# Optimization experiments

Measured on AMD Instinct MI355X. Metric: run time of the kernel, lower is better.

The kernel has to match this reference:

```python
import jax, jax.numpy as jnp
import numpy as np

B, S, L = 4, 1024, 128
H, D = 16, 64            # num_attention_heads, attention_head_size
HID = H * D              # 1024
MAX_POS = 1024


def setup_inputs() -> dict:
    key = jax.random.key(0)
    ks = jax.random.split(key, 12)
    sc = 1.0 / np.sqrt(HID)
    return {
        "hidden_states": jax.random.normal(ks[0], (B, S, HID), jnp.float32),
        "attention_mask": jnp.zeros((B, 1, 1, S), jnp.float32),
        "instruct_hidden_states": jax.random.normal(ks[1], (B, L, HID), jnp.float32),
        "instruct_attention_mask": jnp.zeros((B, 1, 1, L), jnp.float32),
        "Wq": jax.random.normal(ks[2], (HID, HID), jnp.float32) * sc,
        "bq": jnp.zeros((HID,), jnp.float32),
        "Wk": jax.random.normal(ks[3], (HID, HID), jnp.float32) * sc,
        "bk": jnp.zeros((HID,), jnp.float32),
        "Wv": jax.random.normal(ks[4], (HID, HID), jnp.float32) * sc,
        "bv": jnp.zeros((HID,), jnp.float32),
        "gate": jnp.zeros((1, H, 1, 1), jnp.float32),
        "dist_emb": jax.random.normal(ks[5], (2 * MAX_POS - 1, D), jnp.float32) * 0.02,
    }


def _heads(x):
    # [B,T,HID] -> [B,H,T,D]
    b, t, _ = x.shape
    return x.reshape(b, t, H, D).transpose(0, 2, 1, 3)


def reference(hidden_states, attention_mask, instruct_hidden_states,
              instruct_attention_mask, Wq, bq, Wk, bk, Wv, bv, gate, dist_emb):
    inv_sqrt_d = 1.0 / jnp.sqrt(jnp.asarray(D, hidden_states.dtype))

    q = _heads(hidden_states @ Wq + bq)            # [B,H,S,D]
    k = _heads(hidden_states @ Wk + bk)
    v = _heads(hidden_states @ Wv + bv)
    ik = _heads(instruct_hidden_states @ Wk + bk)  # [B,H,L,D]
    iv = _heads(instruct_hidden_states @ Wv + bv)

    scores = jnp.einsum('bhld,bhrd->bhlr', q, k)   # [B,H,S,S]

    # relative_key_query positional scores
    pos = jnp.arange(S)
    dist_idx = pos[:, None] - pos[None, :] + MAX_POS - 1   # [S,S]
    pe = dist_emb[dist_idx]                                # [S,S,D]
    scores = scores + jnp.einsum('bhld,lrd->bhlr', q, pe) \
                    + jnp.einsum('bhrd,lrd->bhlr', k, pe)

    scores = scores * inv_sqrt_d + attention_mask
    probs = jax.nn.softmax(scores, axis=-1)
    ctx = jnp.einsum('bhlr,bhrd->bhld', probs, v)          # [B,H,S,D]

    # gated instruction attention
    iscores = jnp.einsum('bhld,bhrd->bhlr', q, ik) * inv_sqrt_d + instruct_attention_mask
    iprobs = jax.nn.softmax(iscores, axis=-1)
    ictx = jnp.einsum('bhlr,bhrd->bhld', iprobs, iv)
    ctx = ctx + jnp.tanh(gate) * ictx

    # [B,H,S,D] -> [B,S,HID]
    return ctx.transpose(0, 2, 1, 3).reshape(B, S, HID)
```

## Files before the change

### kernel.cpp

```cpp
#include <hip/hip_runtime.h>
#include <cmath>

#define NB 4
#define NH 16
#define SD 64
#define SEQ 1024
#define ILEN 128
#define HIDDIM 1024

#define N_HID (NB*SEQ*HIDDIM)
#define N_INS (NB*ILEN*HIDDIM)
#define N_E_SRC (2047*SD)
#define N_E   (2048*SD)
#define N_W   (HIDDIM*HIDDIM)

typedef short bf8 __attribute__((ext_vector_type(8)));
typedef short bf4 __attribute__((ext_vector_type(4)));
typedef float f4  __attribute__((ext_vector_type(4)));

#define MFMA(a,b,c) __builtin_amdgcn_mfma_f32_16x16x32_bf16(a,b,c,0,0,0)

__device__ __forceinline__ float bf2f(short s) {
    unsigned u = ((unsigned)(unsigned short)s) << 16;
    return __uint_as_float(u);
}
__device__ __forceinline__ short f2bf(float x) {
    unsigned u = __float_as_uint(x);
    u = (u + 0x7FFFu + ((u >> 16) & 1u)) >> 16;
    return (short)u;
}
__device__ __forceinline__ short f2bf_t(float x) {
    return (short)(__float_as_uint(x) >> 16);
}

__global__ __launch_bounds__(256) void cast_flat(
    const float* __restrict__ hid, const float* __restrict__ ins,
    const float* __restrict__ E, short* __restrict__ ws)
{
    int i = (blockIdx.x * 256 + threadIdx.x) * 4;
    short* dhid = ws;
    short* dins = ws + N_HID;
    short* dE   = ws + N_HID + N_INS;
    if (i < N_HID) {
        float4 v = *(const float4*)&hid[i];
        bf4 o; o[0]=f2bf(v.x); o[1]=f2bf(v.y); o[2]=f2bf(v.z); o[3]=f2bf(v.w);
        *(bf4*)&dhid[i] = o;
    } else if (i < N_HID + N_INS) {
        int j = i - N_HID;
        float4 v = *(const float4*)&ins[j];
        bf4 o; o[0]=f2bf(v.x); o[1]=f2bf(v.y); o[2]=f2bf(v.z); o[3]=f2bf(v.w);
        *(bf4*)&dins[j] = o;
    } else {
        int j = i - N_HID - N_INS;
        if (j < N_E) {
            bf4 o;
            if (j < N_E_SRC) {
                float4 v = *(const float4*)&E[j];
                o[0]=f2bf(v.x); o[1]=f2bf(v.y); o[2]=f2bf(v.z); o[3]=f2bf(v.w);
            } else {
                o[0]=0; o[1]=0; o[2]=0; o[3]=0;
            }
            *(bf4*)&dE[j] = o;
        }
    }
}

__global__ __launch_bounds__(256) void cast_wt(
    const float* __restrict__ Wq, const float* __restrict__ Wk,
    const float* __restrict__ Wv, short* __restrict__ dstbase)
{
    const float* W = (blockIdx.z==0) ? Wq : (blockIdx.z==1) ? Wk : Wv;
    short* dst = dstbase + (size_t)blockIdx.z * N_W;
    const int k0 = blockIdx.y*64, n0 = blockIdx.x*64;
    __shared__ float st[64][65];
    const int tid = threadIdx.x;
    #pragma unroll
    for (int rep=0; rep<4; rep++) {
        int u = tid + rep*256;
        int row = u >> 4, col = (u & 15) * 4;
        float4 v = *(const float4*)&W[(size_t)(k0+row)*HIDDIM + n0 + col];
        st[row][col+0]=v.x; st[row][col+1]=v.y; st[row][col+2]=v.z; st[row][col+3]=v.w;
    }
    __syncthreads();
    #pragma unroll
    for (int rep=0; rep<4; rep++) {
        int u = tid + rep*256;
        int nrow = u >> 4, kc = (u & 15) * 4;
        bf4 o;
        #pragma unroll
        for (int j=0;j<4;j++) o[j] = f2bf(st[kc+j][nrow]);
        *(bf4*)&dst[(size_t)(n0+nrow)*HIDDIM + k0 + kc] = o;
    }
}

__global__ __launch_bounds__(256) void proj_mfma(
    const short* __restrict__ hidb, const short* __restrict__ insb,
    const short* __restrict__ WTall,
    const float* __restrict__ bq, const float* __restrict__ bk, const float* __restrict__ bv,
    short* __restrict__ qo, short* __restrict__ ko, short* __restrict__ vTo,
    short* __restrict__ iko, short* __restrict__ ivTo)
{
    const int z = blockIdx.z;
    const int bx = blockIdx.x, by = blockIdx.y;
    if (z==1 && (bx>=16 || by>=4)) return;
    const short* X = z ? insb : hidb;
    const int T   = z ? ILEN : SEQ;
    const int tsh = z ? 7 : 10;
    const int zoff= z ? 1024 : 0;
    const int m0 = by*128, n0 = bx*128;

    __shared__ short Xs[128*72];
    __shared__ short Ws[128*72];

    const int tid=threadIdx.x, w=tid>>6, lane=tid&63, quad=lane>>4, nl=lane&15;
    const int wr = w>>1, wc = w&1;

    f4 acc[4][4];
    #pragma unroll
    for (int ti=0;ti<4;ti++)
      #pragma unroll
      for (int tj=0;tj<4;tj++) { acc[ti][tj][0]=0.f; acc[ti][tj][1]=0.f; acc[ti][tj][2]=0.f; acc[ti][tj][3]=0.f; }

    for (int k0=0; k0<HIDDIM; k0+=64) {
        __syncthreads();
        #pragma unroll
        for (int rep=0; rep<4; rep++) {
            int u = tid + rep*256;
            int row = u >> 3, ch = u & 7;
            *(uint4*)&Xs[row*72 + ch*8] = *(const uint4*)&X[(size_t)(m0+row)*HIDDIM + k0 + ch*8];
            *(uint4*)&Ws[row*72 + ch*8] = *(const uint4*)&WTall[(size_t)(zoff+n0+row)*HIDDIM + k0 + ch*8];
        }
        __syncthreads();
        bf8 a[4][2], b[4][2];
        #pragma unroll
        for (int ti=0;ti<4;ti++)
          #pragma unroll
          for (int s=0;s<2;s++)
            a[ti][s] = *(const bf8*)&Xs[(64*wr + 16*ti + nl)*72 + s*32 + quad*8];
        #pragma unroll
        for (int tj=0;tj<4;tj++)
          #pragma unroll
          for (int s=0;s<2;s++)
            b[tj][s] = *(const bf8*)&Ws[(64*wc + 16*tj + nl)*72 + s*32 + quad*8];
        #pragma unroll
        for (int ti=0;ti<4;ti++)
          #pragma unroll
          for (int tj=0;tj<4;tj++)
            #pragma unroll
            for (int s=0;s<2;s++)
              acc[ti][tj] = MFMA(a[ti][s], b[tj][s], acc[ti][tj]);
    }

    #pragma unroll
    for (int tj=0;tj<4;tj++) {
        const int n = n0 + 64*wc + 16*tj + nl;
        const int nn = n & 1023;
        const int h = nn >> 6, d = nn & 63;
        float bias; short* outp; int mode;
        if (z==0) {
            if (n < 1024)      { bias = bq[nn]; outp = qo;  mode=0; }
            else if (n < 2048) { bias = bk[nn]; outp = ko;  mode=0; }
            else               { bias = bv[nn]; outp = vTo; mode=1; }
        } else {
            if (n < 1024)      { bias = bk[nn]; outp = iko;  mode=0; }
            else               { bias = bv[nn]; outp = ivTo; mode=1; }
        }
        #pragma unroll
        for (int ti=0;ti<4;ti++) {
            const int mb = m0 + 64*wr + 16*ti + quad*4;
            const int bb = mb >> tsh, tt = mb & (T-1);
            if (mode) {
                bf4 o;
                #pragma unroll
                for (int i=0;i<4;i++) o[i] = f2bf(acc[ti][tj][i] + bias);
                *(bf4*)&outp[((size_t)(bb*NH + h)*SD + d)*T + tt] = o;
            } else {
                #pragma unroll
                for (int i=0;i<4;i++)
                    outp[((size_t)(bb*NH + h)*T + tt + i)*SD + d] = f2bf(acc[ti][tj][i] + bias);
            }
        }
    }
}

__global__ __launch_bounds__(256,2) void attn_mfma(
    const short* __restrict__ qg, const short* __restrict__ kg, const short* __restrict__ vTg,
    const short* __restrict__ ikg, const short* __restrict__ ivTg,
    const float* __restrict__ mask, const float* __restrict__ imask,
    const float* __restrict__ gate, const short* __restrict__ Ebf,
    float* __restrict__ out)
{
    const int l0 = blockIdx.x * 64, h = blockIdx.y, b = blockIdx.z;
    const int tid = threadIdx.x, w = tid>>6, lane = tid&63, quad = lane>>4, nl = lane&15;

    __shared__ short ksh[64*72];
    __shared__ short vts[64*72];
    __shared__ short es [128*72];
    __shared__ short qeT[128*68];
    __shared__ short keT[128*68];
    __shared__ short ps [64*72];
    __shared__ float maskS[64];

    const size_t bh = (size_t)(b*NH + h);
    const short* kbase   = kg   + bh*SEQ*SD;
    const short* vTbase  = vTg  + bh*SD*SEQ;
    const short* ikbase  = ikg  + bh*ILEN*SD;
    const short* ivTbase = ivTg + bh*SD*ILEN;

    bf8 aq[2];
    {
        const short* qrow = qg + (bh*SEQ + l0 + 16*w + nl)*SD;
        #pragma unroll
        for (int s=0;s<2;s++) aq[s] = *(const bf8*)&qrow[s*32 + quad*8];
    }

    f4 o1[4], o2[4];
    float m1[4], l1[4], m2[4], l2[4];
    #pragma unroll
    for (int t=0;t<4;t++) {
        o1[t][0]=0.f;o1[t][1]=0.f;o1[t][2]=0.f;o1[t][3]=0.f;
        o2[t][0]=0.f;o2[t][1]=0.f;o2[t][2]=0.f;o2[t][3]=0.f;
        m1[t]=-1e30f; l1[t]=0.f; m2[t]=-1e30f; l2[t]=0.f;
    }

    for (int r0=0; r0<SEQ; r0+=64) {
        const int jb = l0 - r0 + 960;
        __syncthreads();
        #pragma unroll
        for (int rep=0; rep<2; rep++) {
            int u = tid + rep*256;
            int row = u >> 3, ch = u & 7;
            *(uint4*)&ksh[row*72 + ch*8] = *(const uint4*)&kbase[(size_t)(r0+row)*SD + ch*8];
            *(uint4*)&vts[row*72 + ch*8] = *(const uint4*)&vTbase[(size_t)row*SEQ + r0 + ch*8];
        }
        if (r0 == 0) {
            #pragma unroll
            for (int rep=0; rep<4; rep++) {
                int u = tid + rep*256;
                int roff = u >> 3, ch = u & 7;
                int g = jb + roff;
                *(uint4*)&es[(g & 127)*72 + ch*8] = *(const uint4*)&Ebf[(size_t)g*SD + ch*8];
            }
        } else {
            #pragma unroll
            for (int rep=0; rep<2; rep++) {
                int u = tid + rep*256;
                int roff = u >> 3, ch = u & 7;
                int g = jb + roff;
                *(uint4*)&es[(g & 127)*72 + ch*8] = *(const uint4*)&Ebf[(size_t)g*SD + ch*8];
            }
        }
        if (tid < 64) maskS[tid] = mask[b*SEQ + r0 + tid];
        __syncthreads();

        bf8 ak[2];
        #pragma unroll
        for (int s=0;s<2;s++) ak[s] = *(const bf8*)&ksh[(16*w+nl)*72 + s*32 + quad*8];
        f4 sc[4];
        #pragma unroll
        for (int t=0;t<4;t++) { sc[t][0]=0.f; sc[t][1]=0.f; sc[t][2]=0.f; sc[t][3]=0.f; }
        #pragma unroll
        for (int t=0;t<4;t++)
            #pragma unroll
            for (int s=0;s<2;s++) {
                bf8 bk = *(const bf8*)&ksh[(16*t+nl)*72 + s*32 + quad*8];
                sc[t] = MFMA(aq[s], bk, sc[t]);
            }
        f4 qe[5], ke[5];
        #pragma unroll
        for (int j=0;j<5;j++) {
            qe[j][0]=0.f;qe[j][1]=0.f;qe[j][2]=0.f;qe[j][3]=0.f;
            ke[j][0]=0.f;ke[j][1]=0.f;ke[j][2]=0.f;ke[j][3]=0.f;
        }
        #pragma unroll
        for (int j=0;j<5;j++) {
            const int sq = (jb + 16*(w+j)   + nl) & 127;
            const int sk = (jb + 16*(3-w+j) + nl) & 127;
            #pragma unroll
            for (int s=0;s<2;s++) {
                bf8 beq = *(const bf8*)&es[sq*72 + s*32 + quad*8];
                bf8 bek = *(const bf8*)&es[sk*72 + s*32 + quad*8];
                qe[j] = MFMA(aq[s], beq, qe[j]);
                ke[j] = MFMA(ak[s], bek, ke[j]);
            }
        }
        #pragma unroll
        for (int j=0;j<5;j++) {
            bf4 pq, pk;
            #pragma unroll
            for (int i=0;i<4;i++) { pq[i]=f2bf_t(qe[j][i]); pk[i]=f2bf_t(ke[j][i]); }
            *(bf4*)&qeT[(16*(w+j)+nl)*68 + 16*w + quad*4]   = pq;
            *(bf4*)&keT[(16*(3-w+j)+nl)*68 + 16*w + quad*4] = pk;
        }
        __syncthreads();

        float sval[4][4];
        #pragma unroll
        for (int t=0;t<4;t++) {
            const int ri = 16*t + nl;
            const float mk = maskS[ri];
            #pragma unroll
            for (int i=0;i<4;i++) {
                const int li = 16*w + quad*4 + i;
                const int c = li - ri + 63;
                float add = bf2f(qeT[c*68 + li]) + bf2f(keT[c*68 + ri]);
                sval[i][t] = (sc[t][i] + add)*0.125f + mk;
            }
        }
        short pbf[4][4];
        #pragma unroll
        for (int i=0;i<4;i++) {
            float mx = fmaxf(fmaxf(sval[i][0],sval[i][1]), fmaxf(sval[i][2],sval[i][3]));
            #pragma unroll
            for (int off=1; off<16; off<<=1) mx = fmaxf(mx, __shfl_xor(mx, off));
            const float mn = fmaxf(m1[i], mx);
            const float alpha = __expf(m1[i]-mn);
            m1[i] = mn;
            float rs = 0.f;
            #pragma unroll
            for (int t=0;t<4;t++) {
                float p = __expf(sval[i][t]-mn);
                pbf[i][t] = f2bf(p);
                rs += p;
            }
            #pragma unroll
            for (int off=1; off<16; off<<=1) rs += __shfl_xor(rs, off);
            l1[i] = l1[i]*alpha + rs;
            #pragma unroll
            for (int t=0;t<4;t++) o1[t][i] *= alpha;
        }
        #pragma unroll
        for (int i=0;i<4;i++) {
            const int li = 16*w + quad*4 + i;
            #pragma unroll
            for (int t=0;t<4;t++) ps[li*72 + 16*t + nl] = pbf[i][t];
        }
        #pragma unroll
        for (int s=0;s<2;s++) {
            bf8 ap = *(const bf8*)&ps[(16*w+nl)*72 + s*32 + quad*8];
            #pragma unroll
            for (int t=0;t<4;t++) {
                bf8 bv = *(const bf8*)&vts[(16*t+nl)*72 + s*32 + quad*8];
                o1[t] = MFMA(ap, bv, o1[t]);
            }
        }
    }

    for (int r0=0; r0<ILEN; r0+=64) {
        __syncthreads();
        #pragma unroll
        for (int rep=0; rep<2; rep++) {
            int u = tid + rep*256;
            int row = u >> 3, ch = u & 7;
            *(uint4*)&ksh[row*72 + ch*8] = *(const uint4*)&ikbase[(size_t)(r0+row)*SD + ch*8];
            *(uint4*)&vts[row*72 + ch*8] = *(const uint4*)&ivTbase[(size_t)row*ILEN + r0 + ch*8];
        }
        __syncthreads();

        f4 sc[4];
        #pragma unroll
        for (int t=0;t<4;t++) { sc[t][0]=0.f; sc[t][1]=0.f; sc[t][2]=0.f; sc[t][3]=0.f; }
        #pragma unroll
        for (int t=0;t<4;t++)
            #pragma unroll
            for (int s=0;s<2;s++) {
                bf8 bk = *(const bf8*)&ksh[(16*t+nl)*72 + s*32 + quad*8];
                sc[t] = MFMA(aq[s], bk, sc[t]);
            }
        float sval[4][4];
        #pragma unroll
        for (int t=0;t<4;t++) {
            const float mk = imask[b*ILEN + r0 + 16*t + nl];
            #pragma unroll
            for (int i=0;i<4;i++) sval[i][t] = sc[t][i]*0.125f + mk;
        }
        short pbf[4][4];
        #pragma unroll
        for (int i=0;i<4;i++) {
            float mx = fmaxf(fmaxf(sval[i][0],sval[i][1]), fmaxf(sval[i][2],sval[i][3]));
            #pragma unroll
            for (int off=1; off<16; off<<=1) mx = fmaxf(mx, __shfl_xor(mx, off));
            const float mn = fmaxf(m2[i], mx);
            const float alpha = __expf(m2[i]-mn);
            m2[i] = mn;
            float rs = 0.f;
            #pragma unroll
            for (int t=0;t<4;t++) {
                float p = __expf(sval[i][t]-mn);
                pbf[i][t] = f2bf(p);
                rs += p;
            }
            #pragma unroll
            for (int off=1; off<16; off<<=1) rs += __shfl_xor(rs, off);
            l2[i] = l2[i]*alpha + rs;
            #pragma unroll
            for (int t=0;t<4;t++) o2[t][i] *= alpha;
        }
        #pragma unroll
        for (int i=0;i<4;i++) {
            const int li = 16*w + quad*4 + i;
            #pragma unroll
            for (int t=0;t<4;t++) ps[li*72 + 16*t + nl] = pbf[i][t];
        }
        #pragma unroll
        for (int s=0;s<2;s++) {
            bf8 ap = *(const bf8*)&ps[(16*w+nl)*72 + s*32 + quad*8];
            #pragma unroll
            for (int t=0;t<4;t++) {
                bf8 bv = *(const bf8*)&vts[(16*t+nl)*72 + s*32 + quad*8];
                o2[t] = MFMA(ap, bv, o2[t]);
            }
        }
    }

    const float tg = tanhf(gate[h]);
    #pragma unroll
    for (int i=0;i<4;i++) {
        const int l = l0 + 16*w + quad*4 + i;
        const float inv1 = 1.0f/l1[i], inv2 = 1.0f/l2[i];
        #pragma unroll
        for (int t=0;t<4;t++) {
            const int d = 16*t + nl;
            out[((size_t)(b*SEQ + l)*NH + h)*SD + d] = o1[t][i]*inv1 + tg*(o2[t][i]*inv2);
        }
    }
}

extern "C" void kernel_launch(void* const* d_in, const int* in_sizes, int n_in,
                              void* d_out, int out_size, void* d_ws, size_t ws_size,
                              hipStream_t stream) {
    const float* hidden  = (const float*)d_in[0];
    const float* mask    = (const float*)d_in[1];
    const float* ihidden = (const float*)d_in[2];
    const float* imask   = (const float*)d_in[3];
    const float* Wq   = (const float*)d_in[4];
    const float* bq   = (const float*)d_in[5];
    const float* Wk   = (const float*)d_in[6];
    const float* bk   = (const float*)d_in[7];
    const float* Wv   = (const float*)d_in[8];
    const float* bv   = (const float*)d_in[9];
    const float* gate = (const float*)d_in[10];
    const float* dist = (const float*)d_in[11];
    float* out = (float*)d_out;

    short* ws = (short*)d_ws;
    const size_t OFF_INS = N_HID;
    const size_t OFF_E   = OFF_INS + N_INS;
    const size_t OFF_WT  = OFF_E + N_E;
    const size_t OFF_Q   = OFF_WT + 3*(size_t)N_W;
    const size_t OFF_K   = OFF_Q + N_HID;
    const size_t OFF_VT  = OFF_K + N_HID;
    const size_t OFF_IK  = OFF_VT + N_HID;
    const size_t OFF_IVT = OFF_IK + N_INS;

    cast_flat<<<4736, 256, 0, stream>>>(hidden, ihidden, dist, ws);
    cast_wt<<<dim3(16,16,3), 256, 0, stream>>>(Wq, Wk, Wv, ws + OFF_WT);
    proj_mfma<<<dim3(24,32,2), 256, 0, stream>>>(
        ws, ws + OFF_INS, ws + OFF_WT,
        bq, bk, bv,
        ws + OFF_Q, ws + OFF_K, ws + OFF_VT, ws + OFF_IK, ws + OFF_IVT);
    attn_mfma<<<dim3(16,16,4), 256, 0, stream>>>(
        ws + OFF_Q, ws + OFF_K, ws + OFF_VT, ws + OFF_IK, ws + OFF_IVT,
        mask, imask, gate, ws + OFF_E, out);
}
```

Before: 277.6 us.

## Gather query-position scores via lane shuffles and alias LDS buffers to cut shared memory

The query-side relative-position term is now taken straight from MFMA accumulator registers with cross-lane shuffles, so the qeT shared-memory transpose buffer is no longer written or read. The probability buffers reuse the ksh and es regions, and the attention mask is loaded from global memory into registers, which removes maskS. Together these shrink LDS use per block, which may allow more resident blocks, and cut LDS traffic. The cost is extra shuffle and select instructions, and buffer aliasing that depends on the existing barrier ordering being correct. The key-side term now uses round-to-nearest bf16 conversion instead of truncation.

Measured after the change: 275.2 us. Within noise of the previous version (-0.9%).

```diff
diff --git a/kernel.cpp b/kernel.cpp
--- a/kernel.cpp
+++ b/kernel.cpp
@@ -28,9 +28,6 @@
     unsigned u = __float_as_uint(x);
     u = (u + 0x7FFFu + ((u >> 16) & 1u)) >> 16;
     return (short)u;
-}
-__device__ __forceinline__ short f2bf_t(float x) {
-    return (short)(__float_as_uint(x) >> 16);
 }
 
 __global__ __launch_bounds__(256) void cast_flat(
@@ -193,13 +190,12 @@
     const int l0 = blockIdx.x * 64, h = blockIdx.y, b = blockIdx.z;
     const int tid = threadIdx.x, w = tid>>6, lane = tid&63, quad = lane>>4, nl = lane&15;
 
+    __shared__ short keT[128*68];
     __shared__ short ksh[64*72];
     __shared__ short vts[64*72];
     __shared__ short es [128*72];
-    __shared__ short qeT[128*68];
-    __shared__ short keT[128*68];
-    __shared__ short ps [64*72];
-    __shared__ float maskS[64];
+    short* ps  = ksh;
+    short* psi = es;
 
     const size_t bh = (size_t)(b*NH + h);
     const short* kbase   = kg   + bh*SEQ*SD;
@@ -223,6 +219,14 @@
         m1[t]=-1e30f; l1[t]=0.f; m2[t]=-1e30f; l2[t]=0.f;
     }
 
+    int srci[4]; bool ci[4];
+    #pragma unroll
+    for (int i=0;i<4;i++) {
+        const int d0 = 4*quad + i - nl;
+        srci[i] = (lane & 48) | ((d0 - 1) & 15);
+        ci[i]   = (d0 >= 1);
+    }
+
     for (int r0=0; r0<SEQ; r0+=64) {
         const int jb = l0 - r0 + 960;
         __syncthreads();
@@ -250,7 +254,6 @@
                 *(uint4*)&es[(g & 127)*72 + ch*8] = *(const uint4*)&Ebf[(size_t)g*SD + ch*8];
             }
         }
-        if (tid < 64) maskS[tid] = mask[b*SEQ + r0 + tid];
         __syncthreads();
 
         bf8 ak[2];
@@ -284,27 +287,33 @@
                 ke[j] = MFMA(ak[s], bek, ke[j]);
             }
         }
-        #pragma unroll
-        for (int j=0;j<5;j++) {
-            bf4 pq, pk;
-            #pragma unroll
-            for (int i=0;i<4;i++) { pq[i]=f2bf_t(qe[j][i]); pk[i]=f2bf_t(ke[j][i]); }
-            *(bf4*)&qeT[(16*(w+j)+nl)*68 + 16*w + quad*4]   = pq;
-            *(bf4*)&keT[(16*(3-w+j)+nl)*68 + 16*w + quad*4] = pk;
-        }
+        {
+            const int rb = 16*w + 4*quad;
+            #pragma unroll
+            for (int j=0;j<5;j++) {
+                const int c = 16*(3-w+j) + nl;
+                bf4 pk;
+                #pragma unroll
+                for (int i=0;i<4;i++) pk[i] = f2bf(ke[j][i]);
+                *(bf4*)&keT[c*68 + rb] = pk;
+            }
+        }
+        float mk[4];
+        #pragma unroll
+        for (int t=0;t<4;t++) mk[t] = mask[b*SEQ + r0 + 16*t + nl];
         __syncthreads();
 
         float sval[4][4];
         #pragma unroll
-        for (int t=0;t<4;t++) {
-            const int ri = 16*t + nl;
-            const float mk = maskS[ri];
-            #pragma unroll
-            for (int i=0;i<4;i++) {
-                const int li = 16*w + quad*4 + i;
-                const int c = li - ri + 63;
-                float add = bf2f(qeT[c*68 + li]) + bf2f(keT[c*68 + ri]);
-                sval[i][t] = (sc[t][i] + add)*0.125f + mk;
+        for (int i=0;i<4;i++) {
+            const int li = 16*w + 4*quad + i;
+            #pragma unroll
+            for (int t=0;t<4;t++) {
+                float v = ci[i] ? qe[4-t][i] : qe[3-t][i];
+                const float qadd = __shfl(v, srci[i]);
+                const int ri = 16*t + nl;
+                const float kadd = bf2f(keT[(li - ri + 63)*68 + ri]);
+                sval[i][t] = (sc[t][i] + qadd + kadd)*0.125f + mk[t];
             }
         }
         short pbf[4][4];
@@ -370,9 +379,9 @@
         float sval[4][4];
         #pragma unroll
         for (int t=0;t<4;t++) {
-            const float mk = imask[b*ILEN + r0 + 16*t + nl];
-            #pragma unroll
-            for (int i=0;i<4;i++) sval[i][t] = sc[t][i]*0.125f + mk;
+            const float mkv = imask[b*ILEN + r0 + 16*t + nl];
+            #pragma unroll
+            for (int i=0;i<4;i++) sval[i][t] = sc[t][i]*0.125f + mkv;
         }
         short pbf[4][4];
         #pragma unroll
@@ -400,11 +409,11 @@
         for (int i=0;i<4;i++) {
             const int li = 16*w + quad*4 + i;
             #pragma unroll
-            for (int t=0;t<4;t++) ps[li*72 + 16*t + nl] = pbf[i][t];
+            for (int t=0;t<4;t++) psi[li*72 + 16*t + nl] = pbf[i][t];
         }
         #pragma unroll
         for (int s=0;s<2;s++) {
-            bf8 ap = *(const bf8*)&ps[(16*w+nl)*72 + s*32 + quad*8];
+            bf8 ap = *(const bf8*)&psi[(16*w+nl)*72 + s*32 + quad*8];
             #pragma unroll
             for (int t=0;t<4;t++) {
                 bf8 bv = *(const bf8*)&vts[(16*t+nl)*72 + s*32 + quad*8];
```
